# Kernel optimization log

Measured on AMD Instinct MI355X. Metric: run time of the kernel, lower is better.

## Reference

```python
import jax, jax.numpy as jnp
import numpy as np

NEG = -1000000000.0

def setup_inputs() -> dict:
    key = jax.random.key(0)
    k1, k2, k3, k4, k5, k6 = jax.random.split(key, 6)
    B, T, H = 32, 4096, 512
    scale = 1.0 / np.sqrt(H)
    return {
        "enc_seq": jax.random.normal(k1, (B, T, H), dtype=jnp.float32),
        "enc_mask": jax.random.randint(k2, (B, T), 0, 2, dtype=jnp.int32),
        "dec_state": jax.random.normal(k3, (B, H), dtype=jnp.float32),
        "W_h": jax.random.normal(k4, (H, H), dtype=jnp.float32) * scale,
        "W_s": jax.random.normal(k5, (H, H), dtype=jnp.float32) * scale,
        "v": jax.random.normal(k6, (H,), dtype=jnp.float32) * scale,
    }

def reference(enc_seq, enc_mask, dec_state, W_h, W_s, v):
    # torch nn.Linear computes x @ W.T; weights here stored as (out, in) = (H, H)
    h = jnp.einsum("bth,oh->bto", enc_seq, W_h)          # [B,T,H]
    s = jnp.einsum("bh,oh->bo", dec_state, W_s)[:, None]  # [B,1,H]
    e = jnp.einsum("bth,h->bt", jnp.tanh(h + s), v)       # [B,T]
    e = jnp.where(enc_mask == 0, NEG, e)
    a = jax.nn.softmax(e, axis=1)                          # [B,T]
    ctx = jnp.einsum("bt,bth->bh", a, enc_seq)             # [B,H]
    return ctx
```

## Files before the change

### kernel.cpp

```cpp
#include <hip/hip_runtime.h>
#include <hip/hip_bf16.h>

#define B_ 32
#define T_ 4096
#define H_ 512
#define NEGV (-1000000000.0f)
#define LOG2E 1.4426950408889634f

using bf16x8  = __attribute__((ext_vector_type(8))) __bf16;
using short8  = __attribute__((ext_vector_type(8))) short;
using f32x4   = __attribute__((ext_vector_type(4))) float;

static __device__ __forceinline__ short f2bf(float f) {
    unsigned u = __builtin_bit_cast(unsigned, f);
    unsigned r = (u + 0x7fffu + ((u >> 16) & 1u)) >> 16;
    return (short)r;
}

static __device__ __forceinline__ float tanh_fast(float x) {
    float e = __builtin_amdgcn_exp2f(x * 2.8853900817779268f);
    return 1.0f - 2.0f * __builtin_amdgcn_rcpf(e + 1.0f);
}

static __device__ __forceinline__ f32x4 mfma16(short8 a, short8 b, f32x4 c) {
    return __builtin_amdgcn_mfma_f32_16x16x32_bf16(
        __builtin_bit_cast(bf16x8, a), __builtin_bit_cast(bf16x8, b), c, 0, 0, 0);
}

#define GLOAD_LDS16(g, l)                                                     \
    __builtin_amdgcn_global_load_lds(                                         \
        (const __attribute__((address_space(1))) unsigned*)(g),               \
        (__attribute__((address_space(3))) unsigned*)(l), 16, 0, 0)

__global__ __launch_bounds__(256) void wh_prep(const float* __restrict__ Wh,
                                               short* __restrict__ Whp) {
    int id = blockIdx.x * 256 + threadIdx.x;
    int c   = id >> 10;
    int rem = id & 1023;
    int ks  = rem >> 6;
    int l   = rem & 63;
    int n  = c * 16 + (l & 15);
    int k0 = ks * 32 + (l >> 4) * 8;
    const float4* src = (const float4*)(Wh + (size_t)n * H_ + k0);
    float4 f0 = src[0];
    float4 f1 = src[1];
    short8 t;
    t[0] = f2bf(f0.x); t[1] = f2bf(f0.y); t[2] = f2bf(f0.z); t[3] = f2bf(f0.w);
    t[4] = f2bf(f1.x); t[5] = f2bf(f1.y); t[6] = f2bf(f1.z); t[7] = f2bf(f1.w);
    *(short8*)(Whp + (size_t)id * 8) = t;
}

__global__ __launch_bounds__(256) void s_kernel(const float* __restrict__ dec,
                                                const float* __restrict__ Ws,
                                                float* __restrict__ s_out) {
    __shared__ float dec_l[H_];
    int b = blockIdx.y;
    int tid = threadIdx.x;
    dec_l[tid]       = dec[b * H_ + tid];
    dec_l[tid + 256] = dec[b * H_ + tid + 256];
    __syncthreads();
    int o = blockIdx.x * 256 + tid;
    const float4* w = (const float4*)(Ws + (size_t)o * H_);
    float acc = 0.f;
#pragma unroll 8
    for (int k = 0; k < H_ / 4; ++k) {
        float4 wv = w[k];
        acc += wv.x * dec_l[4 * k] + wv.y * dec_l[4 * k + 1] +
               wv.z * dec_l[4 * k + 2] + wv.w * dec_l[4 * k + 3];
    }
    s_out[b * H_ + o] = acc;
}

__global__ __launch_bounds__(256, 2) void e_fused(const float* __restrict__ enc,
                                                  const int* __restrict__ mask,
                                                  const short* __restrict__ Whp,
                                                  const float* __restrict__ s_in,
                                                  const float* __restrict__ v,
                                                  float* __restrict__ pctx,
                                                  float* __restrict__ ml) {
    __shared__ short lds_b[2][16 * 512];
    __shared__ float s_l[H_];
    __shared__ float v_l[H_];
    __shared__ float e_l[64];

    const int tid  = threadIdx.x;
    const int wave = tid >> 6;
    const int lane = tid & 63;
    const int q    = lane >> 4;
    const int lq   = lane & 15;

    const int row0 = blockIdx.x * 64;
    const int b    = row0 >> 12;

    for (int i = tid; i < H_; i += 256) {
        s_l[i] = s_in[b * H_ + i];
        v_l[i] = v[i];
    }

    short8 afrag[16];
    {
        int m = row0 + wave * 16 + lq;
        const float* ap = enc + (size_t)m * H_ + q * 8;
#pragma unroll
        for (int ks = 0; ks < 16; ++ks) {
            float4 f0 = *(const float4*)(ap + ks * 32);
            float4 f1 = *(const float4*)(ap + ks * 32 + 4);
            short8 t;
            t[0] = f2bf(f0.x); t[1] = f2bf(f0.y); t[2] = f2bf(f0.z); t[3] = f2bf(f0.w);
            t[4] = f2bf(f1.x); t[5] = f2bf(f1.y); t[6] = f2bf(f1.z); t[7] = f2bf(f1.w);
            afrag[ks] = t;
        }
    }

    {
        const char* gsrc = (const char*)Whp;
#pragma unroll
        for (int j = 0; j < 4; ++j) {
            int off = wave * 4096 + j * 1024;
            GLOAD_LDS16(gsrc + off + lane * 16, (char*)lds_b[0] + off);
        }
    }

    float e_acc[4] = {};
    __syncthreads();

    for (int nt = 0; nt < 32; ++nt) {
        if (nt < 31) {
            const char* gsrc = (const char*)Whp + (nt + 1) * 16384;
            short* dst = lds_b[(nt + 1) & 1];
#pragma unroll
            for (int j = 0; j < 4; ++j) {
                int off = wave * 4096 + j * 1024;
                GLOAD_LDS16(gsrc + off + lane * 16, (char*)dst + off);
            }
        }
        const short* fp = lds_b[nt & 1] + lane * 8;
        f32x4 acc = {0.f, 0.f, 0.f, 0.f};
#pragma unroll
        for (int ks = 0; ks < 16; ++ks) {
            short8 bf = *(const short8*)(fp + (ks << 9));
            acc = mfma16(afrag[ks], bf, acc);
        }
        int n = nt * 16 + lq;
        float sv = s_l[n];
        float vv = v_l[n];
#pragma unroll
        for (int r = 0; r < 4; ++r)
            e_acc[r] += tanh_fast(acc[r] + sv) * vv;
        __syncthreads();
    }

#pragma unroll
    for (int r = 0; r < 4; ++r) {
        float t = e_acc[r];
        t += __shfl_xor(t, 1, 16);
        t += __shfl_xor(t, 2, 16);
        t += __shfl_xor(t, 4, 16);
        t += __shfl_xor(t, 8, 16);
        if (lq == 0) {
            int mr = wave * 16 + q * 4 + r;
            e_l[mr] = mask[row0 + mr] ? t : NEGV;
        }
    }
    __syncthreads();

    if (wave == 0) {
        float x = e_l[lane];
        float m = x;
#pragma unroll
        for (int off = 32; off > 0; off >>= 1)
            m = fmaxf(m, __shfl_xor(m, off, 64));
        float p = __builtin_amdgcn_exp2f((x - m) * LOG2E);
        float sm = p;
#pragma unroll
        for (int off = 32; off > 0; off >>= 1)
            sm += __shfl_xor(sm, off, 64);
        e_l[lane] = p;
        if (lane == 0) {
            ml[blockIdx.x * 2]     = m;
            ml[blockIdx.x * 2 + 1] = sm;
        }
    }
    __syncthreads();

    const float2* ep = (const float2*)(enc + (size_t)row0 * H_) + tid;
    float2 acc2 = {0.f, 0.f};
#pragma unroll 8
    for (int t = 0; t < 64; ++t) {
        float w = e_l[t];
        float2 v2 = ep[(size_t)t * 256];
        acc2.x += w * v2.x;
        acc2.y += w * v2.y;
    }
    ((float2*)(pctx + (size_t)blockIdx.x * 512))[tid] = acc2;
}

__global__ __launch_bounds__(256) void combine_kernel(const float* __restrict__ pctx,
                                                      const float* __restrict__ ml,
                                                      float* __restrict__ out) {
    int b = blockIdx.x, tid = threadIdx.x;
    const float* mlb = ml + b * 128;
    float M = -3.4e38f;
#pragma unroll
    for (int j = 0; j < 64; ++j) M = fmaxf(M, mlb[2 * j]);
    const float2* pc = (const float2*)(pctx + (size_t)b * 64 * 512) + tid;
    float denom = 0.f;
    float2 acc = {0.f, 0.f};
#pragma unroll
    for (int j = 0; j < 64; ++j) {
        float w = __builtin_amdgcn_exp2f((mlb[2 * j] - M) * LOG2E);
        denom += w * mlb[2 * j + 1];
        float2 p2 = pc[j * 256];
        acc.x += w * p2.x;
        acc.y += w * p2.y;
    }
    float inv = 1.0f / denom;
    float2 o;
    o.x = acc.x * inv;
    o.y = acc.y * inv;
    ((float2*)(out + b * H_))[tid] = o;
}

extern "C" void kernel_launch(void* const* d_in, const int* in_sizes, int n_in,
                              void* d_out, int out_size, void* d_ws, size_t ws_size,
                              hipStream_t stream) {
    (void)in_sizes; (void)n_in; (void)ws_size; (void)out_size;
    const float* enc  = (const float*)d_in[0];
    const int*   mask = (const int*)d_in[1];
    const float* dec  = (const float*)d_in[2];
    const float* Wh   = (const float*)d_in[3];
    const float* Ws   = (const float*)d_in[4];
    const float* v    = (const float*)d_in[5];
    float* out = (float*)d_out;

    short* whp_buf = (short*)d_ws;
    float* s_buf   = (float*)(whp_buf + 512 * 512);
    float* pctx    = s_buf + B_ * H_;
    float* ml      = pctx + 2048 * 512;

    wh_prep<<<dim3(128), 256, 0, stream>>>(Wh, whp_buf);
    s_kernel<<<dim3(2, B_), 256, 0, stream>>>(dec, Ws, s_buf);
    e_fused<<<dim3(B_ * T_ / 64), 256, 0, stream>>>(enc, mask, whp_buf, s_buf, v,
                                                    pctx, ml);
    combine_kernel<<<dim3(B_), 256, 0, stream>>>(pctx, ml, out);
}
```

Baseline: 516.7 us.

## Restructure e_fused loop to stream A in K-quarters with accumulators across N halves

```diff
diff --git a/kernel.cpp b/kernel.cpp
--- a/kernel.cpp
+++ b/kernel.cpp
@@ -35,12 +35,16 @@
 __global__ __launch_bounds__(256) void wh_prep(const float* __restrict__ Wh,
                                                short* __restrict__ Whp) {
     int id = blockIdx.x * 256 + threadIdx.x;
-    int c   = id >> 10;
-    int rem = id & 1023;
-    int ks  = rem >> 6;
-    int l   = rem & 63;
-    int n  = c * 16 + (l & 15);
-    int k0 = ks * 32 + (l >> 4) * 8;
+    int P   = id >> 9;
+    int idx = id & 511;
+    int h  = P >> 5;
+    int q  = (P >> 3) & 3;
+    int nc = P & 7;
+    int s  = idx >> 8;
+    int ks = (idx >> 6) & 3;
+    int l  = idx & 63;
+    int n  = h * 256 + nc * 32 + s * 16 + (l & 15);
+    int k0 = q * 128 + ks * 32 + (l >> 4) * 8;
     const float4* src = (const float4*)(Wh + (size_t)n * H_ + k0);
     float4 f0 = src[0];
     float4 f1 = src[1];
@@ -71,14 +75,16 @@
     s_out[b * H_ + o] = acc;
 }
 
-__global__ __launch_bounds__(256, 2) void e_fused(const float* __restrict__ enc,
-                                                  const int* __restrict__ mask,
-                                                  const short* __restrict__ Whp,
-                                                  const float* __restrict__ s_in,
-                                                  const float* __restrict__ v,
-                                                  float* __restrict__ pctx,
-                                                  float* __restrict__ ml) {
-    __shared__ short lds_b[2][16 * 512];
+__global__ __launch_bounds__(256)
+__attribute__((amdgpu_waves_per_eu(2, 2)))
+void e_fused(const float* __restrict__ enc,
+             const int* __restrict__ mask,
+             const short* __restrict__ Whp,
+             const float* __restrict__ s_in,
+             const float* __restrict__ v,
+             float* __restrict__ pctx,
+             float* __restrict__ ml) {
+    __shared__ short lds_b[2][8192];
     __shared__ float s_l[H_];
     __shared__ float v_l[H_];
     __shared__ float e_l[64];
@@ -86,7 +92,7 @@
     const int tid  = threadIdx.x;
     const int wave = tid >> 6;
     const int lane = tid & 63;
-    const int q    = lane >> 4;
+    const int q4   = lane >> 4;
     const int lq   = lane & 15;
 
     const int row0 = blockIdx.x * 64;
@@ -97,57 +103,109 @@
         v_l[i] = v[i];
     }
 
-    short8 afrag[16];
+    const int arow = row0 + wave * 16 + lq;
+    const float* abase = enc + (size_t)arow * H_ + q4 * 8;
+
     {
-        int m = row0 + wave * 16 + lq;
-        const float* ap = enc + (size_t)m * H_ + q * 8;
-#pragma unroll
-        for (int ks = 0; ks < 16; ++ks) {
-            float4 f0 = *(const float4*)(ap + ks * 32);
-            float4 f1 = *(const float4*)(ap + ks * 32 + 4);
-            short8 t;
-            t[0] = f2bf(f0.x); t[1] = f2bf(f0.y); t[2] = f2bf(f0.z); t[3] = f2bf(f0.w);
-            t[4] = f2bf(f1.x); t[5] = f2bf(f1.y); t[6] = f2bf(f1.z); t[7] = f2bf(f1.w);
-            afrag[ks] = t;
-        }
-    }
-
-    {
-        const char* gsrc = (const char*)Whp;
+        const char* g = (const char*)Whp;
 #pragma unroll
         for (int j = 0; j < 4; ++j) {
             int off = wave * 4096 + j * 1024;
-            GLOAD_LDS16(gsrc + off + lane * 16, (char*)lds_b[0] + off);
-        }
-    }
-
+            GLOAD_LDS16(g + off + lane * 16, (char*)lds_b[0] + off);
+        }
+    }
+
+    float4 fbuf[8];
+#pragma unroll
+    for (int ks = 0; ks < 4; ++ks) {
+        fbuf[2 * ks]     = *(const float4*)(abase + ks * 32);
+        fbuf[2 * ks + 1] = *(const float4*)(abase + ks * 32 + 4);
+    }
+    short8 afrag[4];
+#pragma unroll
+    for (int ks = 0; ks < 4; ++ks) {
+        short8 t;
+        t[0] = f2bf(fbuf[2 * ks].x);     t[1] = f2bf(fbuf[2 * ks].y);
+        t[2] = f2bf(fbuf[2 * ks].z);     t[3] = f2bf(fbuf[2 * ks].w);
+        t[4] = f2bf(fbuf[2 * ks + 1].x); t[5] = f2bf(fbuf[2 * ks + 1].y);
+        t[6] = f2bf(fbuf[2 * ks + 1].z); t[7] = f2bf(fbuf[2 * ks + 1].w);
+        afrag[ks] = t;
+    }
+
+    f32x4 acc[8][2];
+#pragma unroll
+    for (int nc = 0; nc < 8; ++nc)
+#pragma unroll
+        for (int s = 0; s < 2; ++s)
+#pragma unroll
+            for (int z = 0; z < 4; ++z) acc[nc][s][z] = 0.f;
     float e_acc[4] = {};
+
     __syncthreads();
 
-    for (int nt = 0; nt < 32; ++nt) {
-        if (nt < 31) {
-            const char* gsrc = (const char*)Whp + (nt + 1) * 16384;
-            short* dst = lds_b[(nt + 1) & 1];
-#pragma unroll
-            for (int j = 0; j < 4; ++j) {
-                int off = wave * 4096 + j * 1024;
-                GLOAD_LDS16(gsrc + off + lane * 16, (char*)dst + off);
+#pragma unroll
+    for (int Q = 0; Q < 8; ++Q) {
+        const int hh = Q >> 2;
+        const int qq = Q & 3;
+#pragma unroll
+        for (int st = 0; st < 4; ++st) {
+            const int g = Q * 4 + st;
+            if (g < 31) {
+                const char* gs = (const char*)Whp + (size_t)(g + 1) * 16384;
+                short* dst = lds_b[(g + 1) & 1];
+#pragma unroll
+                for (int j = 0; j < 4; ++j) {
+                    int off = wave * 4096 + j * 1024;
+                    GLOAD_LDS16(gs + off + lane * 16, (char*)dst + off);
+                }
             }
-        }
-        const short* fp = lds_b[nt & 1] + lane * 8;
-        f32x4 acc = {0.f, 0.f, 0.f, 0.f};
-#pragma unroll
-        for (int ks = 0; ks < 16; ++ks) {
-            short8 bf = *(const short8*)(fp + (ks << 9));
-            acc = mfma16(afrag[ks], bf, acc);
-        }
-        int n = nt * 16 + lq;
-        float sv = s_l[n];
-        float vv = v_l[n];
-#pragma unroll
-        for (int r = 0; r < 4; ++r)
-            e_acc[r] += tanh_fast(acc[r] + sv) * vv;
-        __syncthreads();
+            if (st == 1 && Q < 7) {
+                const float* ap = abase + ((Q + 1) & 3) * 128;
+#pragma unroll
+                for (int ks = 0; ks < 4; ++ks) {
+                    fbuf[2 * ks]     = *(const float4*)(ap + ks * 32);
+                    fbuf[2 * ks + 1] = *(const float4*)(ap + ks * 32 + 4);
+                }
+            }
+#pragma unroll
+            for (int pc = 0; pc < 2; ++pc) {
+                const int nc = st * 2 + pc;
+                const short* fp = lds_b[g & 1] + pc * 4096 + lane * 8;
+#pragma unroll
+                for (int s = 0; s < 2; ++s) {
+#pragma unroll
+                    for (int ks = 0; ks < 4; ++ks) {
+                        short8 bf = *(const short8*)(fp + (s * 4 + ks) * 512);
+                        acc[nc][s] = mfma16(afrag[ks], bf, acc[nc][s]);
+                    }
+                }
+                if (qq == 3) {
+#pragma unroll
+                    for (int s = 0; s < 2; ++s) {
+                        int n = hh * 256 + nc * 32 + s * 16 + lq;
+                        float sv = s_l[n];
+                        float vv = v_l[n];
+#pragma unroll
+                        for (int r = 0; r < 4; ++r)
+                            e_acc[r] += tanh_fast(acc[nc][s][r] + sv) * vv;
+#pragma unroll
+                        for (int z = 0; z < 4; ++z) acc[nc][s][z] = 0.f;
+                    }
+                }
+            }
+            __syncthreads();
+        }
+        if (Q < 7) {
+#pragma unroll
+            for (int ks = 0; ks < 4; ++ks) {
+                short8 t;
+                t[0] = f2bf(fbuf[2 * ks].x);     t[1] = f2bf(fbuf[2 * ks].y);
+                t[2] = f2bf(fbuf[2 * ks].z);     t[3] = f2bf(fbuf[2 * ks].w);
+                t[4] = f2bf(fbuf[2 * ks + 1].x); t[5] = f2bf(fbuf[2 * ks + 1].y);
+                t[6] = f2bf(fbuf[2 * ks + 1].z); t[7] = f2bf(fbuf[2 * ks + 1].w);
+                afrag[ks] = t;
+            }
+        }
     }
 
 #pragma unroll
@@ -158,7 +216,7 @@
         t += __shfl_xor(t, 4, 16);
         t += __shfl_xor(t, 8, 16);
         if (lq == 0) {
-            int mr = wave * 16 + q * 4 + r;
+            int mr = wave * 16 + q4 * 4 + r;
             e_l[mr] = mask[row0 + mr] ? t : NEGV;
         }
     }
```

Measured after the change: 591.8 us. 14.5% more time.
